# Kernel optimization log

Hardware: AMD Instinct MI355X
Metric: run time of the kernel (lower is better)

The kernel has to match this reference:

```python
import jax, jax.numpy as jnp
import numpy as np

# --- module constants (from init_kwargs) ---
R_HRS = 1000000.0   # high-resistance state (ohm)
R_LRS = 1000.0      # low-resistance state (ohm)
PARASITIC_R = 2.0   # wire resistance per crossbar segment (ohm)
BITS = 4            # conductance quantization bits
BATCH, IN_F, OUT_F = 8192, 1024, 1024


def weight_mapping(W, R_hrs, R_lrs):
    # linearly map weights into the [G_hrs, G_lrs] conductance window
    G_hrs, G_lrs = 1.0 / R_hrs, 1.0 / R_lrs
    Wmin, Wmax = W.min(), W.max()
    return (W - Wmin) / (Wmax - Wmin) * (G_lrs - G_hrs) + G_hrs


def quantization(G, R_lrs, R_hrs, bits):
    # snap conductances to 2**bits uniform levels in [G_hrs, G_lrs]
    G_hrs, G_lrs = 1.0 / R_hrs, 1.0 / R_lrs
    step = (G_lrs - G_hrs) / (2 ** bits - 1)
    return jnp.round((G - G_hrs) / step) * step + G_hrs


def ideal_model(G, x, parasitic_r):
    # ideal crossbar: I = V @ G  (no IR drop)
    return x @ G


def jeong_model(G, x, parasitic_r):
    # Jeong-style analytical IR-drop model: each cell (i, j) sees an extra
    # series wire resistance r*((j+1) segments along its word line +
    # (rows - i) segments along its bit line).
    rows, cols = G.shape  # [in, out]
    r_series = parasitic_r * (
        (jnp.arange(cols, dtype=G.dtype) + 1.0)[None, :]
        + (rows - jnp.arange(rows, dtype=G.dtype))[:, None]
    )  # [in, out]
    G_eff = 1.0 / (1.0 / G + r_series)
    return x @ G_eff  # [batch, out]


def output_unmapping(Wt, currents, x, R_hrs, R_lrs):
    # invert the affine conductance mapping: G = a*W + b  =>  x@W = (I - b*sum(x))/a
    G_hrs, G_lrs = 1.0 / R_hrs, 1.0 / R_lrs
    Wmin, Wmax = Wt.min(), Wt.max()
    a = (G_lrs - G_hrs) / (Wmax - Wmin)
    b = G_hrs - a * Wmin
    return (currents - b * x.sum(axis=1, keepdims=True)) / a


def setup_inputs() -> dict:
    key = jax.random.key(0)
    k1, k2, k3 = jax.random.split(key, 3)
    x = jax.random.uniform(k1, (BATCH, IN_F), dtype=jnp.float32)          # read voltages in [0,1)
    weight = jax.random.normal(k2, (OUT_F, IN_F), dtype=jnp.float32) * 0.1
    bias = jax.random.normal(k3, (OUT_F,), dtype=jnp.float32) * 0.01
    return {"x": x, "weight": weight, "bias": bias}


def reference(x, weight, bias):
    Wt = weight.T  # [in, out], matches self.weight.T in the torch module
    conductances = quantization(weight_mapping(Wt, R_HRS, R_LRS), R_LRS, R_HRS, BITS)
    currents = jeong_model(conductances, x, PARASITIC_R)          # non-ideal simulation
    ideal_currents = ideal_model(conductances, x, PARASITIC_R)    # bias-correction pass
    correction = currents.mean(axis=1) / ideal_currents.mean(axis=1)  # [batch]
    output = output_unmapping(Wt, currents, x, R_HRS, R_LRS)      # [batch, out]
    return output + bias[None, :] * correction[:, None]
```

## Files before the change

### kernel.cpp

```cpp
#include <hip/hip_runtime.h>
#include <hip/hip_bf16.h>
#include <cstdint>

#define BATCH 8192
#define IN_F  1024
#define OUT_F 1024
#define G_HRS 1e-6f
#define G_LRS 1e-3f
#define PAR_R 2.0f
#define LEVELS 15.0f

#define WS_PMIN  0
#define WS_PMAX  1024
#define WS_VEFF  4096
#define WS_VID   8192
#define WS_CORR  16384
#define WS_BT    65536
#define WS_ABF   (65536 + 2097152)
#define WS_NEED_FULL  ((size_t)WS_ABF + (size_t)BATCH * IN_F * 2)

__device__ __forceinline__ unsigned short f2bf(float f) {
    union { float f; unsigned int i; } v; v.f = f;
    unsigned int u = v.i;
    unsigned int r = (u + 0x7FFFu + ((u >> 16) & 1u)) >> 16;
    return (unsigned short)r;
}
__device__ __forceinline__ float quant_g(float wv, float wmin, float inv_range) {
    float t = (wv - wmin) * inv_range;
    float step = (G_LRS - G_HRS) / LEVELS;
    return rintf(t * LEVELS) * step + G_HRS;
}

__global__ void kprep(const float* __restrict__ w, float* __restrict__ pmin, float* __restrict__ pmax,
                      float* __restrict__ veff, float* __restrict__ vid) {
    int tid = blockIdx.x * blockDim.x + threadIdx.x;
    float lo = 1e30f, hi = -1e30f;
    const float4* w4 = (const float4*)w;
    const int n4 = (IN_F * OUT_F) / 4;
    for (int i = tid; i < n4; i += 256 * 256) {
        float4 q = w4[i];
        lo = fminf(lo, fminf(fminf(q.x, q.y), fminf(q.z, q.w)));
        hi = fmaxf(hi, fmaxf(fmaxf(q.x, q.y), fmaxf(q.z, q.w)));
    }
#pragma unroll
    for (int m = 1; m < 64; m <<= 1) {
        lo = fminf(lo, __shfl_xor(lo, m, 64));
        hi = fmaxf(hi, __shfl_xor(hi, m, 64));
    }
    __shared__ float slo[4], shi[4];
    int wv = threadIdx.x >> 6, ln = threadIdx.x & 63;
    if (ln == 0) { slo[wv] = lo; shi[wv] = hi; }
    __syncthreads();
    if (threadIdx.x == 0) {
        pmin[blockIdx.x] = fminf(fminf(slo[0], slo[1]), fminf(slo[2], slo[3]));
        pmax[blockIdx.x] = fmaxf(fmaxf(shi[0], shi[1]), fmaxf(shi[2], shi[3]));
    }
    if (blockIdx.x == 0) {
        float4 z = make_float4(0.f, 0.f, 0.f, 0.f);
        ((float4*)veff)[threadIdx.x] = z;
        ((float4*)vid)[threadIdx.x]  = z;
    }
}

__global__ void kbuildvec(const float* __restrict__ w, const float* __restrict__ pmin,
                          const float* __restrict__ pmax, unsigned short* __restrict__ bt,
                          float* __restrict__ veff, float* __restrict__ vid) {
    float lo = pmin[threadIdx.x], hi = pmax[threadIdx.x];
#pragma unroll
    for (int m = 1; m < 64; m <<= 1) {
        lo = fminf(lo, __shfl_xor(lo, m, 64));
        hi = fmaxf(hi, __shfl_xor(hi, m, 64));
    }
    __shared__ float slo[4], shi[4];
    int wv = threadIdx.x >> 6, ln = threadIdx.x & 63;
    if (ln == 0) { slo[wv] = lo; shi[wv] = hi; }
    __syncthreads();
    float wmin = fminf(fminf(slo[0], slo[1]), fminf(slo[2], slo[3]));
    float wmax = fmaxf(fmaxf(shi[0], shi[1]), fmaxf(shi[2], shi[3]));

    float inv_range = 1.0f / (wmax - wmin);
    float acoef = (G_LRS - G_HRS) * inv_range;
    float bcoef = G_HRS - acoef * wmin;
    float inva = 1.0f / acoef;

    int k0 = threadIdx.x * 4;
    float se[4] = {0.f, 0.f, 0.f, 0.f}, si[4] = {0.f, 0.f, 0.f, 0.f};
#pragma unroll
    for (int rr = 0; rr < 16; rr++) {
        int n = blockIdx.x * 16 + rr;
        float4 q = *(const float4*)&w[(size_t)n * IN_F + k0];
        float wvv[4] = { q.x, q.y, q.z, q.w };
        unsigned short o[4];
#pragma unroll
        for (int j = 0; j < 4; j++) {
            int k = k0 + j;
            float g = quant_g(wvv[j], wmin, inv_range);
            float r = PAR_R * ((float)(n + 1) + (float)(IN_F - k));
            float ge = 1.0f / (1.0f / g + r);
            o[j] = f2bf((ge - bcoef) * inva);
            se[j] += ge;
            si[j] += g;
        }
        uint2 ov;
        ov.x = (unsigned int)o[0] | ((unsigned int)o[1] << 16);
        ov.y = (unsigned int)o[2] | ((unsigned int)o[3] << 16);
        *(uint2*)&bt[(size_t)n * IN_F + k0] = ov;
    }
#pragma unroll
    for (int j = 0; j < 4; j++) {
        atomicAdd(&veff[k0 + j], se[j]);
        atomicAdd(&vid[k0 + j], si[j]);
    }
}

__global__ void kcorr(const float* __restrict__ x, const float* __restrict__ veff,
                      const float* __restrict__ vid, float* __restrict__ corr,
                      unsigned short* __restrict__ abf) {
    int row = blockIdx.x * 4 + (threadIdx.x >> 6);
    int lane = threadIdx.x & 63;
    int k0 = lane * 16;
    const float* xr = x + (size_t)row * IN_F + k0;
    float se = 0.f, si = 0.f;
#pragma unroll
    for (int p = 0; p < 4; p++) {
        float4 q  = *(const float4*)(xr + p * 4);
        float4 ve = *(const float4*)(veff + k0 + p * 4);
        float4 vi = *(const float4*)(vid  + k0 + p * 4);
        se += q.x * ve.x + q.y * ve.y + q.z * ve.z + q.w * ve.w;
        si += q.x * vi.x + q.y * vi.y + q.z * vi.z + q.w * vi.w;
        if (abf) {
            uint2 ov;
            ov.x = (unsigned int)f2bf(q.x) | ((unsigned int)f2bf(q.y) << 16);
            ov.y = (unsigned int)f2bf(q.z) | ((unsigned int)f2bf(q.w) << 16);
            *(uint2*)&abf[(size_t)row * IN_F + k0 + p * 4] = ov;
        }
    }
#pragma unroll
    for (int m = 1; m < 64; m <<= 1) {
        se += __shfl_xor(se, m, 64);
        si += __shfl_xor(si, m, 64);
    }
    if (lane == 0) corr[row] = se / si;
}

typedef __attribute__((ext_vector_type(8))) short bf16x8;
typedef __attribute__((ext_vector_type(4))) float f32x4;

#define GLD_LDS16(g, l) \
    __builtin_amdgcn_global_load_lds((const __attribute__((address_space(1))) void*)(g), \
                                     (__attribute__((address_space(3))) void*)(l), 16, 0, 0)

#define LGKM0 do { asm volatile("s_waitcnt lgkmcnt(0)" ::: "memory"); \
                   __builtin_amdgcn_sched_barrier(0); } while (0)
#define VMCNT(n) asm volatile("s_waitcnt vmcnt(" #n ")" ::: "memory")
#define SBAR     asm volatile("s_barrier" ::: "memory")

#define MFMA_ROW(MT, A) \
    acc[MT][0] = __builtin_amdgcn_mfma_f32_16x16x32_bf16(A, b0, acc[MT][0], 0, 0, 0); \
    acc[MT][1] = __builtin_amdgcn_mfma_f32_16x16x32_bf16(A, b1, acc[MT][1], 0, 0, 0); \
    acc[MT][2] = __builtin_amdgcn_mfma_f32_16x16x32_bf16(A, b2, acc[MT][2], 0, 0, 0); \
    acc[MT][3] = __builtin_amdgcn_mfma_f32_16x16x32_bf16(A, b3, acc[MT][3], 0, 0, 0);

__global__ __launch_bounds__(256) void kgemm2(
    const unsigned short* __restrict__ Abf,
    const unsigned short* __restrict__ Bt,
    const float* __restrict__ bias,
    const float* __restrict__ corr,
    float* __restrict__ out)
{
    __shared__ unsigned short As[2 * 128 * 64];
    __shared__ unsigned short Bs[2 * 128 * 64];
    const int tid = threadIdx.x;
    const int f = blockIdx.x;
    const int bm = ((f & 7) * 8 + ((f >> 3) & 7)) * 128;
    const int bn = (f >> 6) * 128;
    const int wave = tid >> 6, lane = tid & 63;
    const int wmL = (wave >> 1) * 64;
    const int wnL = (wave & 1) * 64;
    const int fr = lane & 15;
    const int quad = lane >> 4;

    const int sw   = (fr & 7) * 16;
    const int aRd0 = (wmL + fr) * 128 + ((quad * 16) ^ sw);
    const int aRd1 = (wmL + fr) * 128 + (((64 + quad * 16)) ^ sw);
    const int bRd0 = (wnL + fr) * 128 + ((quad * 16) ^ sw);
    const int bRd1 = (wnL + fr) * 128 + (((64 + quad * 16)) ^ sw);

    const int arow  = tid >> 3;
    const int acolb = ((tid & 7) * 16) ^ ((arow & 7) * 16);
    const unsigned short* gA = Abf + (size_t)(bm + arow) * IN_F + (acolb >> 1);
    const unsigned short* gB = Bt  + (size_t)(bn + arow) * IN_F + (acolb >> 1);

    f32x4 acc[4][4] = {};

    {
        unsigned short* lA = As + tid * 8;
        unsigned short* lB = Bs + tid * 8;
        GLD_LDS16(gB,              lB);
        GLD_LDS16(gB + 32 * IN_F,  lB + 2048);
        GLD_LDS16(gB + 64 * IN_F,  lB + 4096);
        GLD_LDS16(gB + 96 * IN_F,  lB + 6144);
        GLD_LDS16(gA,              lA);
        GLD_LDS16(gA + 32 * IN_F,  lA + 2048);
        GLD_LDS16(gA + 64 * IN_F,  lA + 4096);
        GLD_LDS16(gA + 96 * IN_F,  lA + 6144);
        VMCNT(0);
        SBAR;
    }

#pragma unroll 1
    for (int t = 0; t < 15; ++t) {
        const int rb = (t & 1) << 13;
        const int wb = rb ^ 8192;
        const int kbn = t * 64 + 64;
        const char* Ar = (const char*)(As + rb);
        const char* Br = (const char*)(Bs + rb);
        unsigned short* Aw = As + wb + tid * 8;
        unsigned short* Bw = Bs + wb + tid * 8;
        bf16x8 b0, b1, b2, b3, a0, a1;

        b0 = *(const bf16x8*)(Br + bRd0);
        b1 = *(const bf16x8*)(Br + bRd0 + 2048);
        b2 = *(const bf16x8*)(Br + bRd0 + 4096);
        b3 = *(const bf16x8*)(Br + bRd0 + 6144);
        a0 = *(const bf16x8*)(Ar + aRd0);
        a1 = *(const bf16x8*)(Ar + aRd0 + 2048);
        GLD_LDS16(gB + kbn,             Bw);
        GLD_LDS16(gB + 32 * IN_F + kbn, Bw + 2048);
        LGKM0;
        __builtin_amdgcn_s_setprio(1);
        MFMA_ROW(0, a0)
        MFMA_ROW(1, a1)
        __builtin_amdgcn_s_setprio(0);
        __builtin_amdgcn_sched_barrier(0);
        VMCNT(2);
        SBAR;

        a0 = *(const bf16x8*)(Ar + aRd0 + 4096);
        a1 = *(const bf16x8*)(Ar + aRd0 + 6144);
        GLD_LDS16(gB + 64 * IN_F + kbn, Bw + 4096);
        GLD_LDS16(gB + 96 * IN_F + kbn, Bw + 6144);
        LGKM0;
        __builtin_amdgcn_s_setprio(1);
        MFMA_ROW(2, a0)
        MFMA_ROW(3, a1)
        __builtin_amdgcn_s_setprio(0);
        __builtin_amdgcn_sched_barrier(0);

        b0 = *(const bf16x8*)(Br + bRd1);
        b1 = *(const bf16x8*)(Br + bRd1 + 2048);
        b2 = *(const bf16x8*)(Br + bRd1 + 4096);
        b3 = *(const bf16x8*)(Br + bRd1 + 6144);
        a0 = *(const bf16x8*)(Ar + aRd1);
        a1 = *(const bf16x8*)(Ar + aRd1 + 2048);
        GLD_LDS16(gA + kbn,             Aw);
        GLD_LDS16(gA + 64 * IN_F + kbn, Aw + 4096);
        LGKM0;
        __builtin_amdgcn_s_setprio(1);
        MFMA_ROW(0, a0)
        MFMA_ROW(1, a1)
        __builtin_amdgcn_s_setprio(0);
        __builtin_amdgcn_sched_barrier(0);

        a0 = *(const bf16x8*)(Ar + aRd1 + 4096);
        a1 = *(const bf16x8*)(Ar + aRd1 + 6144);
        GLD_LDS16(gA + 32 * IN_F + kbn, Aw + 2048);
        GLD_LDS16(gA + 96 * IN_F + kbn, Aw + 6144);
        LGKM0;
        __builtin_amdgcn_s_setprio(1);
        MFMA_ROW(2, a0)
        MFMA_ROW(3, a1)
        __builtin_amdgcn_s_setprio(0);
        __builtin_amdgcn_sched_barrier(0);
        VMCNT(2);
        SBAR;
    }

    {
        const char* Ar = (const char*)(As + 8192);
        const char* Br = (const char*)(Bs + 8192);
        bf16x8 b0, b1, b2, b3, a0, a1;

        b0 = *(const bf16x8*)(Br + bRd0);
        b1 = *(const bf16x8*)(Br + bRd0 + 2048);
        b2 = *(const bf16x8*)(Br + bRd0 + 4096);
        b3 = *(const bf16x8*)(Br + bRd0 + 6144);
        a0 = *(const bf16x8*)(Ar + aRd0);
        a1 = *(const bf16x8*)(Ar + aRd0 + 2048);
        LGKM0;
        __builtin_amdgcn_s_setprio(1);
        MFMA_ROW(0, a0)
        MFMA_ROW(1, a1)
        __builtin_amdgcn_s_setprio(0);
        __builtin_amdgcn_sched_barrier(0);
        VMCNT(0);
        SBAR;

        a0 = *(const bf16x8*)(Ar + aRd0 + 4096);
        a1 = *(const bf16x8*)(Ar + aRd0 + 6144);
        LGKM0;
        __builtin_amdgcn_s_setprio(1);
        MFMA_ROW(2, a0)
        MFMA_ROW(3, a1)
        __builtin_amdgcn_s_setprio(0);
        __builtin_amdgcn_sched_barrier(0);

        b0 = *(const bf16x8*)(Br + bRd1);
        b1 = *(const bf16x8*)(Br + bRd1 + 2048);
        b2 = *(const bf16x8*)(Br + bRd1 + 4096);
        b3 = *(const bf16x8*)(Br + bRd1 + 6144);
        a0 = *(const bf16x8*)(Ar + aRd1);
        a1 = *(const bf16x8*)(Ar + aRd1 + 2048);
        LGKM0;
        __builtin_amdgcn_s_setprio(1);
        MFMA_ROW(0, a0)
        MFMA_ROW(1, a1)
        __builtin_amdgcn_s_setprio(0);
        __builtin_amdgcn_sched_barrier(0);

        a0 = *(const bf16x8*)(Ar + aRd1 + 4096);
        a1 = *(const bf16x8*)(Ar + aRd1 + 6144);
        LGKM0;
        __builtin_amdgcn_s_setprio(1);
        MFMA_ROW(2, a0)
        MFMA_ROW(3, a1)
        __builtin_amdgcn_s_setprio(0);
        __builtin_amdgcn_sched_barrier(0);
    }

#pragma unroll
    for (int nt = 0; nt < 4; nt++) {
        int gc = bn + wnL + nt * 16 + fr;
        float bv = bias[gc];
#pragma unroll
        for (int mt = 0; mt < 4; mt++) {
#pragma unroll
            for (int r = 0; r < 4; r++) {
                int gr = bm + wmL + mt * 16 + quad * 4 + r;
                out[(size_t)gr * OUT_F + gc] = acc[mt][nt][r] + bv * corr[gr];
            }
        }
    }
}

__global__ __launch_bounds__(256) void kgemm_conva(
    const float* __restrict__ Af32,
    const unsigned short* __restrict__ Bt,
    const float* __restrict__ bias,
    const float* __restrict__ corr,
    float* __restrict__ out)
{
    __shared__ unsigned short As0[128 * 32];
    __shared__ unsigned short As1[128 * 32];
    __shared__ unsigned short Bs0[128 * 32];
    __shared__ unsigned short Bs1[128 * 32];
    const int tid = threadIdx.x;
    const int f = blockIdx.x;
    const int bm = ((f & 7) * 8 + ((f >> 3) & 7)) * 128;
    const int bn = (f >> 6) * 128;
    const int wave = tid >> 6, lane = tid & 63;
    const int wmL = (wave >> 1) * 64;
    const int wnL = (wave & 1) * 64;
    const int fr = lane & 15;
    const int fk = (lane >> 4) * 8;
    const int quad = lane >> 4;

    f32x4 acc[4][4] = {};

    const int c0 = tid, c1 = tid + 256;
    const unsigned short* gB0 = Bt + (size_t)(bn + (c0 >> 2)) * IN_F + ((c0 & 3) << 3);
    const unsigned short* gB1 = Bt + (size_t)(bn + (c1 >> 2)) * IN_F + ((c1 & 3) << 3);
    const float* fA0 = Af32 + (size_t)(bm + (c0 >> 2)) * IN_F + ((c0 & 3) << 3);
    const float* fA1 = Af32 + (size_t)(bm + (c1 >> 2)) * IN_F + ((c1 & 3) << 3);

    for (int kb = 0; kb < IN_F; kb += 64) {
        float4 p[8];
        p[0] = *(const float4*)(fA0 + kb);      p[1] = *(const float4*)(fA0 + kb + 4);
        p[2] = *(const float4*)(fA1 + kb);      p[3] = *(const float4*)(fA1 + kb + 4);
        p[4] = *(const float4*)(fA0 + kb + 32); p[5] = *(const float4*)(fA0 + kb + 36);
        p[6] = *(const float4*)(fA1 + kb + 32); p[7] = *(const float4*)(fA1 + kb + 36);
        uint4 u[4];
#pragma unroll
        for (int j = 0; j < 4; j++) {
            u[j] = make_uint4(
                (unsigned int)f2bf(p[2*j].x) | ((unsigned int)f2bf(p[2*j].y) << 16),
                (unsigned int)f2bf(p[2*j].z) | ((unsigned int)f2bf(p[2*j].w) << 16),
                (unsigned int)f2bf(p[2*j+1].x) | ((unsigned int)f2bf(p[2*j+1].y) << 16),
                (unsigned int)f2bf(p[2*j+1].z) | ((unsigned int)f2bf(p[2*j+1].w) << 16));
        }
        __syncthreads();
        *(uint4*)&As0[c0 * 8] = u[0];
        *(uint4*)&As0[c1 * 8] = u[1];
        *(uint4*)&As1[c0 * 8] = u[2];
        *(uint4*)&As1[c1 * 8] = u[3];
        GLD_LDS16(gB0 + kb, &Bs0[c0 * 8]);
        GLD_LDS16(gB1 + kb, &Bs0[c1 * 8]);
        GLD_LDS16(gB0 + kb + 32, &Bs1[c0 * 8]);
        GLD_LDS16(gB1 + kb + 32, &Bs1[c1 * 8]);
        __syncthreads();

        bf16x8 af[4], bfv[4];
#pragma unroll
        for (int mt = 0; mt < 4; mt++)
            af[mt] = *(const bf16x8*)&As0[(wmL + mt * 16 + fr) * 32 + fk];
#pragma unroll
        for (int nt = 0; nt < 4; nt++)
            bfv[nt] = *(const bf16x8*)&Bs0[(wnL + nt * 16 + fr) * 32 + fk];
#pragma unroll
        for (int mt = 0; mt < 4; mt++)
#pragma unroll
            for (int nt = 0; nt < 4; nt++)
                acc[mt][nt] = __builtin_amdgcn_mfma_f32_16x16x32_bf16(af[mt], bfv[nt], acc[mt][nt], 0, 0, 0);
#pragma unroll
        for (int mt = 0; mt < 4; mt++)
            af[mt] = *(const bf16x8*)&As1[(wmL + mt * 16 + fr) * 32 + fk];
#pragma unroll
        for (int nt = 0; nt < 4; nt++)
            bfv[nt] = *(const bf16x8*)&Bs1[(wnL + nt * 16 + fr) * 32 + fk];
#pragma unroll
        for (int mt = 0; mt < 4; mt++)
#pragma unroll
            for (int nt = 0; nt < 4; nt++)
                acc[mt][nt] = __builtin_amdgcn_mfma_f32_16x16x32_bf16(af[mt], bfv[nt], acc[mt][nt], 0, 0, 0);
    }

#pragma unroll
    for (int nt = 0; nt < 4; nt++) {
        int gc = bn + wnL + nt * 16 + fr;
        float bv = bias[gc];
#pragma unroll
        for (int mt = 0; mt < 4; mt++) {
#pragma unroll
            for (int r = 0; r < 4; r++) {
                int gr = bm + wmL + mt * 16 + quad * 4 + r;
                out[(size_t)gr * OUT_F + gc] = acc[mt][nt][r] + bv * corr[gr];
            }
        }
    }
}

extern "C" void kernel_launch(void* const* d_in, const int* in_sizes, int n_in,
                              void* d_out, int out_size, void* d_ws, size_t ws_size,
                              hipStream_t stream) {
    const float* x    = (const float*)d_in[0];
    const float* w    = (const float*)d_in[1];
    const float* bias = (const float*)d_in[2];
    float* out = (float*)d_out;

    char* ws = (char*)d_ws;
    float* pmin        = (float*)(ws + WS_PMIN);
    float* pmax        = (float*)(ws + WS_PMAX);
    float* veff        = (float*)(ws + WS_VEFF);
    float* vid         = (float*)(ws + WS_VID);
    float* corr        = (float*)(ws + WS_CORR);
    unsigned short* bt = (unsigned short*)(ws + WS_BT);
    unsigned short* abf = (unsigned short*)(ws + WS_ABF);

    bool full = ws_size >= WS_NEED_FULL;

    kprep<<<256, 256, 0, stream>>>(w, pmin, pmax, veff, vid);
    kbuildvec<<<OUT_F / 16, 256, 0, stream>>>(w, pmin, pmax, bt, veff, vid);
    kcorr<<<BATCH / 4, 256, 0, stream>>>(x, veff, vid, corr, full ? abf : nullptr);
    if (full)
        kgemm2<<<512, 256, 0, stream>>>(abf, bt, bias, corr, out);
    else
        kgemm_conva<<<512, 256, 0, stream>>>(x, bt, bias, corr, out);
}
```

Before: 133.6 us.

## Prefetch second k-half LDS fragments early with partial lgkmcnt waits in GEMM loop

```diff
diff --git a/kernel.cpp b/kernel.cpp
--- a/kernel.cpp
+++ b/kernel.cpp
@@ -118,21 +118,21 @@
                       unsigned short* __restrict__ abf) {
     int row = blockIdx.x * 4 + (threadIdx.x >> 6);
     int lane = threadIdx.x & 63;
-    int k0 = lane * 16;
-    const float* xr = x + (size_t)row * IN_F + k0;
+    const float* xr = x + (size_t)row * IN_F;
     float se = 0.f, si = 0.f;
 #pragma unroll
     for (int p = 0; p < 4; p++) {
-        float4 q  = *(const float4*)(xr + p * 4);
-        float4 ve = *(const float4*)(veff + k0 + p * 4);
-        float4 vi = *(const float4*)(vid  + k0 + p * 4);
+        int off = p * 256 + lane * 4;
+        float4 q  = *(const float4*)(xr + off);
+        float4 ve = *(const float4*)(veff + off);
+        float4 vi = *(const float4*)(vid  + off);
         se += q.x * ve.x + q.y * ve.y + q.z * ve.z + q.w * ve.w;
         si += q.x * vi.x + q.y * vi.y + q.z * vi.z + q.w * vi.w;
         if (abf) {
             uint2 ov;
             ov.x = (unsigned int)f2bf(q.x) | ((unsigned int)f2bf(q.y) << 16);
             ov.y = (unsigned int)f2bf(q.z) | ((unsigned int)f2bf(q.w) << 16);
-            *(uint2*)&abf[(size_t)row * IN_F + k0 + p * 4] = ov;
+            *(uint2*)&abf[(size_t)row * IN_F + off] = ov;
         }
     }
 #pragma unroll
@@ -150,16 +150,16 @@
     __builtin_amdgcn_global_load_lds((const __attribute__((address_space(1))) void*)(g), \
                                      (__attribute__((address_space(3))) void*)(l), 16, 0, 0)
 
-#define LGKM0 do { asm volatile("s_waitcnt lgkmcnt(0)" ::: "memory"); \
-                   __builtin_amdgcn_sched_barrier(0); } while (0)
+#define SCHED0   __builtin_amdgcn_sched_barrier(0)
+#define LGKM(n)  do { asm volatile("s_waitcnt lgkmcnt(" #n ")" ::: "memory"); SCHED0; } while (0)
 #define VMCNT(n) asm volatile("s_waitcnt vmcnt(" #n ")" ::: "memory")
 #define SBAR     asm volatile("s_barrier" ::: "memory")
 
-#define MFMA_ROW(MT, A) \
-    acc[MT][0] = __builtin_amdgcn_mfma_f32_16x16x32_bf16(A, b0, acc[MT][0], 0, 0, 0); \
-    acc[MT][1] = __builtin_amdgcn_mfma_f32_16x16x32_bf16(A, b1, acc[MT][1], 0, 0, 0); \
-    acc[MT][2] = __builtin_amdgcn_mfma_f32_16x16x32_bf16(A, b2, acc[MT][2], 0, 0, 0); \
-    acc[MT][3] = __builtin_amdgcn_mfma_f32_16x16x32_bf16(A, b3, acc[MT][3], 0, 0, 0);
+#define MFMA_ROW4(MT, A, B0, B1, B2, B3) \
+    acc[MT][0] = __builtin_amdgcn_mfma_f32_16x16x32_bf16(A, B0, acc[MT][0], 0, 0, 0); \
+    acc[MT][1] = __builtin_amdgcn_mfma_f32_16x16x32_bf16(A, B1, acc[MT][1], 0, 0, 0); \
+    acc[MT][2] = __builtin_amdgcn_mfma_f32_16x16x32_bf16(A, B2, acc[MT][2], 0, 0, 0); \
+    acc[MT][3] = __builtin_amdgcn_mfma_f32_16x16x32_bf16(A, B3, acc[MT][3], 0, 0, 0);
 
 __global__ __launch_bounds__(256) void kgemm2(
     const unsigned short* __restrict__ Abf,
@@ -218,6 +218,8 @@
         unsigned short* Aw = As + wb + tid * 8;
         unsigned short* Bw = Bs + wb + tid * 8;
         bf16x8 b0, b1, b2, b3, a0, a1;
+        bf16x8 c0, c1, c2, c3, p0, p1;
+        bf16x8 q0, q1;
 
         b0 = *(const bf16x8*)(Br + bRd0);
         b1 = *(const bf16x8*)(Br + bRd0 + 2048);
@@ -225,27 +227,87 @@
         b3 = *(const bf16x8*)(Br + bRd0 + 6144);
         a0 = *(const bf16x8*)(Ar + aRd0);
         a1 = *(const bf16x8*)(Ar + aRd0 + 2048);
+        SCHED0;
+        c0 = *(const bf16x8*)(Br + bRd1);
+        c1 = *(const bf16x8*)(Br + bRd1 + 2048);
+        c2 = *(const bf16x8*)(Br + bRd1 + 4096);
+        c3 = *(const bf16x8*)(Br + bRd1 + 6144);
+        p0 = *(const bf16x8*)(Ar + aRd1);
+        p1 = *(const bf16x8*)(Ar + aRd1 + 2048);
         GLD_LDS16(gB + kbn,             Bw);
         GLD_LDS16(gB + 32 * IN_F + kbn, Bw + 2048);
-        LGKM0;
-        __builtin_amdgcn_s_setprio(1);
-        MFMA_ROW(0, a0)
-        MFMA_ROW(1, a1)
-        __builtin_amdgcn_s_setprio(0);
-        __builtin_amdgcn_sched_barrier(0);
+        LGKM(6);
+        __builtin_amdgcn_s_setprio(1);
+        MFMA_ROW4(0, a0, b0, b1, b2, b3)
+        MFMA_ROW4(1, a1, b0, b1, b2, b3)
+        __builtin_amdgcn_s_setprio(0);
+        SCHED0;
         VMCNT(2);
         SBAR;
 
         a0 = *(const bf16x8*)(Ar + aRd0 + 4096);
         a1 = *(const bf16x8*)(Ar + aRd0 + 6144);
+        SCHED0;
+        q0 = *(const bf16x8*)(Ar + aRd1 + 4096);
+        q1 = *(const bf16x8*)(Ar + aRd1 + 6144);
         GLD_LDS16(gB + 64 * IN_F + kbn, Bw + 4096);
         GLD_LDS16(gB + 96 * IN_F + kbn, Bw + 6144);
-        LGKM0;
-        __builtin_amdgcn_s_setprio(1);
-        MFMA_ROW(2, a0)
-        MFMA_ROW(3, a1)
-        __builtin_amdgcn_s_setprio(0);
-        __builtin_amdgcn_sched_barrier(0);
+        LGKM(2);
+        __builtin_amdgcn_s_setprio(1);
+        MFMA_ROW4(2, a0, b0, b1, b2, b3)
+        MFMA_ROW4(3, a1, b0, b1, b2, b3)
+        __builtin_amdgcn_s_setprio(0);
+        SCHED0;
+
+        GLD_LDS16(gA + kbn,             Aw);
+        GLD_LDS16(gA + 64 * IN_F + kbn, Aw + 4096);
+        LGKM(2);
+        __builtin_amdgcn_s_setprio(1);
+        MFMA_ROW4(0, p0, c0, c1, c2, c3)
+        MFMA_ROW4(1, p1, c0, c1, c2, c3)
+        __builtin_amdgcn_s_setprio(0);
+        SCHED0;
+
+        GLD_LDS16(gA + 32 * IN_F + kbn, Aw + 2048);
+        GLD_LDS16(gA + 96 * IN_F + kbn, Aw + 6144);
+        LGKM(0);
+        __builtin_amdgcn_s_setprio(1);
+        MFMA_ROW4(2, q0, c0, c1, c2, c3)
+        MFMA_ROW4(3, q1, c0, c1, c2, c3)
+        __builtin_amdgcn_s_setprio(0);
+        SCHED0;
+        VMCNT(2);
+        SBAR;
+    }
+
+    {
+        const char* Ar = (const char*)(As + 8192);
+        const char* Br = (const char*)(Bs + 8192);
+        bf16x8 b0, b1, b2, b3, a0, a1;
+
+        b0 = *(const bf16x8*)(Br + bRd0);
+        b1 = *(const bf16x8*)(Br + bRd0 + 2048);
+        b2 = *(const bf16x8*)(Br + bRd0 + 4096);
+        b3 = *(const bf16x8*)(Br + bRd0 + 6144);
+        a0 = *(const bf16x8*)(Ar + aRd0);
+        a1 = *(const bf16x8*)(Ar + aRd0 + 2048);
+        LGKM(0);
+        __builtin_amdgcn_s_setprio(1);
+        MFMA_ROW4(0, a0, b0, b1, b2, b3)
+        MFMA_ROW4(1, a1, b0, b1, b2, b3)
+        __builtin_amdgcn_s_setprio(0);
+        SCHED0;
+        VMCNT(0);
+        SBAR;
+
+        a0 = *(const bf16x8*)(Ar + aRd0 + 4096);
+        a1 = *(const bf16x8*)(Ar + aRd0 + 6144);
+        LGKM(0);
+        __builtin_amdgcn_s_setprio(1);
+        MFMA_ROW4(2, a0, b0, b1, b2, b3)
+        MFMA_ROW4(3, a1, b0, b1, b2, b3)
+        __builtin_amdgcn_s_setprio(0);
+        SCHED0;
 
         b0 = *(const bf16x8*)(Br + bRd1);
         b1 = *(const bf16x8*)(Br + bRd1 + 2048);
@@ -253,79 +315,21 @@
         b3 = *(const bf16x8*)(Br + bRd1 + 6144);
         a0 = *(const bf16x8*)(Ar + aRd1);
         a1 = *(const bf16x8*)(Ar + aRd1 + 2048);
-        GLD_LDS16(gA + kbn,             Aw);
-        GLD_LDS16(gA + 64 * IN_F + kbn, Aw + 4096);
-        LGKM0;
-        __builtin_amdgcn_s_setprio(1);
-        MFMA_ROW(0, a0)
-        MFMA_ROW(1, a1)
-        __builtin_amdgcn_s_setprio(0);
-        __builtin_amdgcn_sched_barrier(0);
+        LGKM(0);
+        __builtin_amdgcn_s_setprio(1);
+        MFMA_ROW4(0, a0, b0, b1, b2, b3)
+        MFMA_ROW4(1, a1, b0, b1, b2, b3)
+        __builtin_amdgcn_s_setprio(0);
+        SCHED0;
 
         a0 = *(const bf16x8*)(Ar + aRd1 + 4096);
         a1 = *(const bf16x8*)(Ar + aRd1 + 6144);
-        GLD_LDS16(gA + 32 * IN_F + kbn, Aw + 2048);
-        GLD_LDS16(gA + 96 * IN_F + kbn, Aw + 6144);
-        LGKM0;
-        __builtin_amdgcn_s_setprio(1);
-        MFMA_ROW(2, a0)
-        MFMA_ROW(3, a1)
-        __builtin_amdgcn_s_setprio(0);
-        __builtin_amdgcn_sched_barrier(0);
-        VMCNT(2);
-        SBAR;
-    }
-
-    {
-        const char* Ar = (const char*)(As + 8192);
-        const char* Br = (const char*)(Bs + 8192);
-        bf16x8 b0, b1, b2, b3, a0, a1;
-
-        b0 = *(const bf16x8*)(Br + bRd0);
-        b1 = *(const bf16x8*)(Br + bRd0 + 2048);
-        b2 = *(const bf16x8*)(Br + bRd0 + 4096);
-        b3 = *(const bf16x8*)(Br + bRd0 + 6144);
-        a0 = *(const bf16x8*)(Ar + aRd0);
-        a1 = *(const bf16x8*)(Ar + aRd0 + 2048);
-        LGKM0;
-        __builtin_amdgcn_s_setprio(1);
-        MFMA_ROW(0, a0)
-        MFMA_ROW(1, a1)
-        __builtin_amdgcn_s_setprio(0);
-        __builtin_amdgcn_sched_barrier(0);
-        VMCNT(0);
-        SBAR;
-
-        a0 = *(const bf16x8*)(Ar + aRd0 + 4096);
-        a1 = *(const bf16x8*)(Ar + aRd0 + 6144);
-        LGKM0;
-        __builtin_amdgcn_s_setprio(1);
-        MFMA_ROW(2, a0)
-        MFMA_ROW(3, a1)
-        __builtin_amdgcn_s_setprio(0);
-        __builtin_amdgcn_sched_barrier(0);
-
-        b0 = *(const bf16x8*)(Br + bRd1);
-        b1 = *(const bf16x8*)(Br + bRd1 + 2048);
-        b2 = *(const bf16x8*)(Br + bRd1 + 4096);
-        b3 = *(const bf16x8*)(Br + bRd1 + 6144);
-        a0 = *(const bf16x8*)(Ar + aRd1);
-        a1 = *(const bf16x8*)(Ar + aRd1 + 2048);
-        LGKM0;
-        __builtin_amdgcn_s_setprio(1);
-        MFMA_ROW(0, a0)
-        MFMA_ROW(1, a1)
-        __builtin_amdgcn_s_setprio(0);
-        __builtin_amdgcn_sched_barrier(0);
-
-        a0 = *(const bf16x8*)(Ar + aRd1 + 4096);
-        a1 = *(const bf16x8*)(Ar + aRd1 + 6144);
-        LGKM0;
-        __builtin_amdgcn_s_setprio(1);
-        MFMA_ROW(2, a0)
-        MFMA_ROW(3, a1)
-        __builtin_amdgcn_s_setprio(0);
-        __builtin_amdgcn_sched_barrier(0);
+        LGKM(0);
+        __builtin_amdgcn_s_setprio(1);
+        MFMA_ROW4(2, a0, b0, b1, b2, b3)
+        MFMA_ROW4(3, a1, b0, b1, b2, b3)
+        __builtin_amdgcn_s_setprio(0);
+        SCHED0;
     }
 
 #pragma unroll
```

After: 126.1 us. 1.06x faster.
